# Kernel tuning notes

Measured on AMD Instinct MI355X. Metric: run time of the kernel, lower is better.

## Reference

```python
import jax, jax.numpy as jnp
import numpy as np

N = 100000      # nodes
E = 1600000     # edges
FX = 128        # raw node feature dim
MAXZ = 100      # z embedding / one-hot size
HID = 128       # hidden_channels
NL = 3          # num_layers
G = 512         # num graphs
BN_EPS = 1e-5


def _lin(key, din, dout):
    return jax.random.normal(key, (din, dout), jnp.float32) * (1.0 / np.sqrt(din))


def setup_inputs() -> dict:
    key = jax.random.key(0)
    ks = jax.random.split(key, 64)
    d = {}
    d["x"] = jax.random.normal(ks[0], (N, FX), jnp.float32)
    d["z"] = jax.random.randint(ks[1], (N,), 0, MAXZ)
    d["edge_index"] = jax.random.randint(ks[2], (2, E), 0, N)
    d["batch"] = jnp.sort(jax.random.randint(ks[3], (N,), 0, G))
    in0 = FX + 2 * MAXZ  # z_emb concatenated twice (faithful to source)
    ki = 4
    for l in range(NL):
        din = in0 if l == 0 else HID
        d[f"W1_{l}"] = _lin(ks[ki], din, HID); ki += 1
        d[f"b1_{l}"] = jnp.zeros((HID,), jnp.float32)
        d[f"W2_{l}"] = _lin(ks[ki], HID, HID); ki += 1
        d[f"b2_{l}"] = jnp.zeros((HID,), jnp.float32)
        d[f"g_{l}"] = jnp.ones((HID,), jnp.float32)
        d[f"be_{l}"] = jnp.zeros((HID,), jnp.float32)
    d["Wl1"] = _lin(ks[ki], NL * HID, HID); ki += 1
    d["bl1"] = jnp.zeros((HID,), jnp.float32)
    d["Wl2"] = _lin(ks[ki], HID, 1); ki += 1
    d["bl2"] = jnp.zeros((1,), jnp.float32)
    return d


def _gin_layer(h, src, dst, W1, b1, W2, b2, g, be):
    # GINConv with eps=0: nn(x + sum_{j->i} x_j)
    agg = jax.ops.segment_sum(h[src], dst, num_segments=N)  # [N, d]
    m = h + agg
    m = jax.nn.relu(m @ W1 + b1)
    m = jax.nn.relu(m @ W2 + b2)
    # training-mode BatchNorm1d over node axis (biased variance)
    mu = m.mean(0)
    var = jnp.mean((m - mu) ** 2, axis=0)
    return (m - mu) * jax.lax.rsqrt(var + BN_EPS) * g + be


def reference(x, z, edge_index, batch,
              W1_0, b1_0, W2_0, b2_0, g_0, be_0,
              W1_1, b1_1, W2_1, b2_1, g_1, be_1,
              W1_2, b1_2, W2_2, b2_2, g_2, be_2,
              Wl1, bl1, Wl2, bl2):
    src, dst = edge_index[0], edge_index[1]
    z_emb = jax.nn.one_hot(z, MAXZ, dtype=jnp.float32)  # [N, MAXZ]
    h = jnp.concatenate([z_emb, x], axis=1)
    h = jnp.concatenate([z_emb, h], axis=1)  # faithful double concat -> [N, FX+2*MAXZ]
    params = [(W1_0, b1_0, W2_0, b2_0, g_0, be_0),
              (W1_1, b1_1, W2_1, b2_1, g_1, be_1),
              (W1_2, b1_2, W2_2, b2_2, g_2, be_2)]
    xs = []
    for p in params:
        h = _gin_layer(h, src, dst, *p)
        xs.append(h)
    hcat = jnp.concatenate(xs, axis=1)  # jumping knowledge: [N, NL*HID]
    # global_mean_pool over graph ids
    counts = jax.ops.segment_sum(jnp.ones((N,), jnp.float32), batch, num_segments=G)
    pooled = jax.ops.segment_sum(hcat, batch, num_segments=G) / jnp.maximum(counts, 1.0)[:, None]
    out = jax.nn.relu(pooled @ Wl1 + bl1)
    # dropout is identity in eval / reference mode
    out = out @ Wl2 + bl2  # [G, 1]
    return out
```

## Files before the change

kernel.cpp:

```cpp
#include <hip/hip_runtime.h>
#include <hip/hip_bf16.h>

#define NN 100000
#define NROWS_PAD 100032
#define EE 1600000
#define GG 512
#define NPB 256
#define NB  ((NN + NPB - 1) / NPB)
#define PCHUNK 4096
#define PBLOCKS ((EE + PCHUNK - 1) / PCHUNK)
#define SBANK 8
static constexpr float BN_EPS = 1e-5f;

typedef _Float16 half8 __attribute__((ext_vector_type(8)));
typedef float floatx4 __attribute__((ext_vector_type(4)));


__global__ __launch_bounds__(256) void k_bhist(const int* __restrict__ EI,
                                               int* __restrict__ bcount)
{
    __shared__ int h[NB];
    const int t = threadIdx.x;
    for (int i = t; i < NB; i += 256) h[i] = 0;
    __syncthreads();
    const int e0 = blockIdx.x * PCHUNK;
    const int e1 = (e0 + PCHUNK < EE) ? e0 + PCHUNK : EE;
    for (int e = e0 + t; e < e1; e += 256)
        atomicAdd(&h[EI[EE + e] >> 8], 1);
    __syncthreads();
    for (int i = t; i < NB; i += 256)
        if (h[i]) atomicAdd(&bcount[i], h[i]);
}

__global__ __launch_bounds__(512) void k_bscan(const int* __restrict__ bcount,
                                               int* __restrict__ bstart,
                                               int* __restrict__ bcursor,
                                               int* __restrict__ row_start)
{
    __shared__ int s[512];
    int t = threadIdx.x;
    int v = (t < NB) ? bcount[t] : 0;
    s[t] = v;
    __syncthreads();
    for (int off = 1; off < 512; off <<= 1) {
        int u = (t >= off) ? s[t - off] : 0;
        __syncthreads();
        s[t] += u;
        __syncthreads();
    }
    if (t < NB) { int ex = s[t] - v; bstart[t] = ex; bcursor[t] = ex; }
    if (t == 0) { bstart[NB] = EE; row_start[NN] = EE; }
}

__global__ __launch_bounds__(256) void k_part(const int* __restrict__ EI,
                                              int* __restrict__ bcursor,
                                              int* __restrict__ ebuf)
{
    __shared__ int h[NB];
    __shared__ int cur[NB];
    const int t = threadIdx.x;
    for (int i = t; i < NB; i += 256) h[i] = 0;
    __syncthreads();
    const int e0 = blockIdx.x * PCHUNK;
    const int e1 = (e0 + PCHUNK < EE) ? e0 + PCHUNK : EE;
    for (int e = e0 + t; e < e1; e += 256)
        atomicAdd(&h[EI[EE + e] >> 8], 1);
    __syncthreads();
    for (int i = t; i < NB; i += 256)
        cur[i] = h[i] ? atomicAdd(&bcursor[i], h[i]) : 0;
    __syncthreads();
    for (int e = e0 + t; e < e1; e += 256) {
        int s = EI[e], d = EI[EE + e];
        int pos = atomicAdd(&cur[d >> 8], 1);
        ebuf[pos] = s | ((d & (NPB - 1)) << 17);
    }
}

__global__ __launch_bounds__(256) void k_csrbucket(const int* __restrict__ ebuf,
                                                   const int* __restrict__ bstart,
                                                   int* __restrict__ row_start,
                                                   int* __restrict__ ssrc)
{
    __shared__ int cnt[NPB];
    __shared__ int cur[NPB];
    const int b = blockIdx.x, t = threadIdx.x;
    cnt[t] = 0;
    __syncthreads();
    const int e0 = bstart[b], e1 = bstart[b + 1];
    for (int e = e0 + t; e < e1; e += 256) {
        unsigned p = (unsigned)__builtin_nontemporal_load(&ebuf[e]);
        atomicAdd(&cnt[p >> 17], 1);
    }
    __syncthreads();
    int myc = cnt[t];
    for (int off = 1; off < 256; off <<= 1) {
        int u = (t >= off) ? cnt[t - off] : 0;
        __syncthreads();
        cnt[t] += u;
        __syncthreads();
    }
    int pos0 = e0 + cnt[t] - myc;
    int idx = b * NPB + t;
    if (idx < NN) row_start[idx] = pos0;
    cur[t] = pos0;
    __syncthreads();
    for (int e = e0 + t; e < e1; e += 256) {
        unsigned p = (unsigned)__builtin_nontemporal_load(&ebuf[e]);
        int pos = atomicAdd(&cur[p >> 17], 1);
        ssrc[pos] = (int)(p & 0x1FFFFu);
    }
}


__global__ __launch_bounds__(256) void k_xcast(const float* __restrict__ X,
                                               _Float16* __restrict__ Xh)
{
    int idx = blockIdx.x * 256 + threadIdx.x;
    const float4* src = (const float4*)X;
    float4 a = src[idx * 2], b = src[idx * 2 + 1];
    half8 o = { (_Float16)a.x, (_Float16)a.y, (_Float16)a.z, (_Float16)a.w,
                (_Float16)b.x, (_Float16)b.y, (_Float16)b.z, (_Float16)b.w };
    *(half8*)&Xh[idx * 8] = o;
}

__device__ __forceinline__ void bn_sc_sh(const float* statsL,
                                         const float* g, const float* be, int k,
                                         float& sc, float& sh)
{
    float cs = 0.f, cq = 0.f;
    #pragma unroll
    for (int b = 0; b < SBANK; ++b) {
        cs += statsL[b * 256 + k];
        cq += statsL[b * 256 + 128 + k];
    }
    float inv_n = 1.0f / (float)NN;
    float mu = cs * inv_n;
    float var = cq * inv_n - mu * mu;
    sc = g[k] * rsqrtf(var + BN_EPS);
    sh = be[k] - mu * sc;
}

__global__ __launch_bounds__(256) void k_prep(
    const float* __restrict__ W1, const float* __restrict__ W2,
    const float* __restrict__ statsPrev,
    const float* __restrict__ g, const float* __restrict__ be,
    _Float16* __restrict__ Wt1, _Float16* __restrict__ Wt2,
    float* __restrict__ cvec, int l)
{
    int b = blockIdx.x, t = threadIdx.x;
    if (b < 64) {
        int idx = b * 256 + t;
        int n = idx >> 7, k = idx & 127;
        if (l == 0) {
            Wt1[idx] = (_Float16)W1[(200 + k) * 128 + n];
        } else {
            float sc, sh;
            bn_sc_sh(statsPrev, g, be, k, sc, sh);
            Wt1[idx] = (_Float16)(sc * W1[k * 128 + n]);
        }
    } else if (b < 128) {
        int idx = (b - 64) * 256 + t;
        int n = idx >> 7, k = idx & 127;
        Wt2[idx] = (_Float16)W2[k * 128 + n];
    } else if (t < 128) {
        float acc = 0.f;
        if (l != 0) {
            for (int k = 0; k < 128; ++k) {
                float sc, sh;
                bn_sc_sh(statsPrev, g, be, k, sc, sh);
                acc = fmaf(sh, W1[k * 128 + t], acc);
            }
        }
        cvec[t] = acc;
    }
}


#define MM_CORE_G(Ah, Wth)                                                   \
    const int lane = tid & 63;                                               \
    const int wv = tid >> 6;                                                 \
    const int ml = lane & 15;                                                \
    const int quad = lane >> 4;                                              \
    const int wr = wv >> 1, wc = wv & 1;                                     \
    floatx4 acc[2][4];                                                       \
    for (int r = 0; r < 2; ++r)                                              \
        for (int t = 0; t < 4; ++t)                                          \
            acc[r][t] = (floatx4){0.f, 0.f, 0.f, 0.f};                       \
    {                                                                        \
        const size_t ar0 = (size_t)(row0 + 32 * wr + ml) * 128;              \
        const size_t ar1 = ar0 + (size_t)16 * 128;                           \
        _Pragma("unroll")                                                    \
        for (int kq = 0; kq < 4; ++kq) {                                     \
            int k0 = kq * 32;                                                \
            half8 a0 = *(const half8*)&Ah[ar0 + k0 + quad * 8];              \
            half8 a1 = *(const half8*)&Ah[ar1 + k0 + quad * 8];              \
            _Pragma("unroll")                                                \
            for (int t = 0; t < 4; ++t) {                                    \
                half8 bf = *(const half8*)&Wth[(size_t)(64 * wc + 16 * t + ml) * 128 + k0 + quad * 8]; \
                acc[0][t] = __builtin_amdgcn_mfma_f32_16x16x32_f16(a0, bf, acc[0][t], 0, 0, 0); \
                acc[1][t] = __builtin_amdgcn_mfma_f32_16x16x32_f16(a1, bf, acc[1][t], 0, 0, 0); \
            }                                                                \
        }                                                                    \
    }

__global__ __launch_bounds__(256) void k_mm_embed(
    const _Float16* __restrict__ Ah, const _Float16* __restrict__ Wth,
    const int* __restrict__ Z, const float* __restrict__ W1,
    _Float16* __restrict__ Ph)
{
    const int tid = threadIdx.x;
    const int row0 = blockIdx.x * 64;
    MM_CORE_G(Ah, Wth)
    #pragma unroll
    for (int r = 0; r < 2; ++r)
        #pragma unroll
        for (int j = 0; j < 4; ++j) {
            int grow = row0 + 32 * wr + 16 * r + quad * 4 + j;
            if (grow < NN) {
                int zv = Z[grow];
                const float* w0 = &W1[zv * 128];
                const float* w1 = &W1[(100 + zv) * 128];
                #pragma unroll
                for (int t = 0; t < 4; ++t) {
                    int gcol = 64 * wc + 16 * t + ml;
                    float v = acc[r][t][j] + w0[gcol] + w1[gcol];
                    Ph[(size_t)grow * 128 + gcol] = (_Float16)v;
                }
            }
        }
}

__global__ __launch_bounds__(256) void k_mm1(
    const _Float16* __restrict__ Ah, const _Float16* __restrict__ Wth,
    _Float16* __restrict__ Ph)
{
    const int tid = threadIdx.x;
    const int row0 = blockIdx.x * 64;
    MM_CORE_G(Ah, Wth)
    #pragma unroll
    for (int r = 0; r < 2; ++r)
        #pragma unroll
        for (int j = 0; j < 4; ++j) {
            int grow = row0 + 32 * wr + 16 * r + quad * 4 + j;
            if (grow < NN) {
                #pragma unroll
                for (int t = 0; t < 4; ++t) {
                    int gcol = 64 * wc + 16 * t + ml;
                    Ph[(size_t)grow * 128 + gcol] = (_Float16)acc[r][t][j];
                }
            }
        }
}

__global__ __launch_bounds__(256) void k_mm2(
    const _Float16* __restrict__ Ah, const _Float16* __restrict__ Wth,
    const float* __restrict__ b2, _Float16* __restrict__ Oh,
    float* __restrict__ statsL)
{
    __shared__ float cs[128];
    __shared__ float cq[128];
    const int tid = threadIdx.x;
    const int row0 = blockIdx.x * 64;
    if (tid < 128) { cs[tid] = 0.f; cq[tid] = 0.f; }
    __syncthreads();

    MM_CORE_G(Ah, Wth)

    float b2v[4];
    #pragma unroll
    for (int t = 0; t < 4; ++t) b2v[t] = b2[64 * wc + 16 * t + ml];
    float st[4] = {0.f, 0.f, 0.f, 0.f};
    float qt[4] = {0.f, 0.f, 0.f, 0.f};
    #pragma unroll
    for (int r = 0; r < 2; ++r)
        #pragma unroll
        for (int j = 0; j < 4; ++j) {
            int grow = row0 + 32 * wr + 16 * r + quad * 4 + j;
            if (grow < NN) {
                #pragma unroll
                for (int t = 0; t < 4; ++t) {
                    int gcol = 64 * wc + 16 * t + ml;
                    float v = fmaxf(acc[r][t][j] + b2v[t], 0.f);
                    Oh[(size_t)grow * 128 + gcol] = (_Float16)v;
                    st[t] += v;
                    qt[t] += v * v;
                }
            }
        }
    #pragma unroll
    for (int t = 0; t < 4; ++t) {
        int gcol = 64 * wc + 16 * t + ml;
        atomicAdd(&cs[gcol], st[t]);
        atomicAdd(&cq[gcol], qt[t]);
    }
    __syncthreads();
    if (tid < 128) {
        float* bank = statsL + (blockIdx.x & (SBANK - 1)) * 256;
        atomicAdd(&bank[tid], cs[tid]);
        atomicAdd(&bank[128 + tid], cq[tid]);
    }
}


__global__ __launch_bounds__(256) void k_aggregate(
    const _Float16* __restrict__ Ph, const int* __restrict__ row_start,
    const int* __restrict__ ssrc, const float* __restrict__ b1,
    const float* __restrict__ cvec, _Float16* __restrict__ Mh)
{
    int idx = blockIdx.x * 256 + threadIdx.x;
    int node = idx >> 4, q = idx & 15;
    if (node >= NN) return;
    int s0 = row_start[node], s1 = row_start[node + 1];
    float degp1 = (float)(s1 - s0 + 1);
    float acc[8];
    half8 pv = *(const half8*)&Ph[(size_t)node * 128 + q * 8];
    #pragma unroll
    for (int j = 0; j < 8; ++j)
        acc[j] = (float)pv[j] + fmaf(degp1, cvec[q * 8 + j], b1[q * 8 + j]);
    int e = s0;
    for (; e + 7 < s1; e += 8) {
        int sidx[8];
        #pragma unroll
        for (int u = 0; u < 8; ++u)
            sidx[u] = __builtin_nontemporal_load(&ssrc[e + u]);
        half8 v[8];
        #pragma unroll
        for (int u = 0; u < 8; ++u)
            v[u] = *(const half8*)&Ph[(size_t)sidx[u] * 128 + q * 8];
        #pragma unroll
        for (int j = 0; j < 8; ++j)
            acc[j] += (((float)v[0][j] + (float)v[1][j]) + ((float)v[2][j] + (float)v[3][j]))
                    + (((float)v[4][j] + (float)v[5][j]) + ((float)v[6][j] + (float)v[7][j]));
    }
    for (; e + 1 < s1; e += 2) {
        int sa = __builtin_nontemporal_load(&ssrc[e]);
        int sb = __builtin_nontemporal_load(&ssrc[e + 1]);
        half8 va = *(const half8*)&Ph[(size_t)sa * 128 + q * 8];
        half8 vb = *(const half8*)&Ph[(size_t)sb * 128 + q * 8];
        #pragma unroll
        for (int j = 0; j < 8; ++j) acc[j] += (float)va[j] + (float)vb[j];
    }
    if (e < s1) {
        int sa = __builtin_nontemporal_load(&ssrc[e]);
        half8 va = *(const half8*)&Ph[(size_t)sa * 128 + q * 8];
        #pragma unroll
        for (int j = 0; j < 8; ++j) acc[j] += (float)va[j];
    }
    half8 o;
    #pragma unroll
    for (int j = 0; j < 8; ++j) o[j] = (_Float16)fmaxf(acc[j], 0.f);
    __builtin_nontemporal_store(o, (half8*)&Mh[(size_t)node * 128 + q * 8]);
}


__global__ __launch_bounds__(128) void k_pool(
    const _Float16* __restrict__ Ah, const int* __restrict__ batch,
    const float* __restrict__ statsL,
    const float* __restrict__ g_, const float* __restrict__ be,
    float* __restrict__ pooled, int loff)
{
    __shared__ float red[8][128];
    int g = blockIdx.x;
    int t = threadIdx.x;
    int rg = t >> 4, seg = t & 15;
    int lo = 0, hi = NN;
    while (lo < hi) { int mid = (lo + hi) >> 1; if (batch[mid] < g) lo = mid + 1; else hi = mid; }
    int s = lo;
    lo = s; hi = NN;
    while (lo < hi) { int mid = (lo + hi) >> 1; if (batch[mid] < g + 1) lo = mid + 1; else hi = mid; }
    int e = lo;
    float acc[8] = {};
    for (int i = s + rg; i < e; i += 8) {
        half8 v = *(const half8*)&Ah[(size_t)i * 128 + seg * 8];
        #pragma unroll
        for (int j = 0; j < 8; ++j) acc[j] += (float)v[j];
    }
    #pragma unroll
    for (int j = 0; j < 8; ++j) red[rg][seg * 8 + j] = acc[j];
    __syncthreads();
    int cnt = e - s;
    float inv = 1.0f / (float)(cnt > 0 ? cnt : 1);
    if (t < 128) {
        float s_ = 0.f;
        #pragma unroll
        for (int r = 0; r < 8; ++r) s_ += red[r][t];
        float sc, sh;
        bn_sc_sh(statsL, g_, be, t, sc, sh);
        pooled[g * 384 + loff + t] = fmaf(sc, s_ * inv, sh);
    }
}

__global__ __launch_bounds__(128) void k_final(
    const float* __restrict__ pooled,
    const float* __restrict__ Wl1, const float* __restrict__ bl1,
    const float* __restrict__ Wl2, const float* __restrict__ bl2,
    float* __restrict__ out)
{
    __shared__ float pr[384];
    __shared__ float red[128];
    int g = blockIdx.x, j = threadIdx.x;
    for (int i = j; i < 384; i += 128) pr[i] = pooled[g * 384 + i];
    __syncthreads();
    float acc = bl1[j];
    for (int k = 0; k < 384; ++k) acc = fmaf(pr[k], Wl1[k * 128 + j], acc);
    float r = fmaxf(acc, 0.f) * Wl2[j];
    red[j] = r;
    __syncthreads();
    for (int off = 64; off > 0; off >>= 1) {
        if (j < off) red[j] += red[j + off];
        __syncthreads();
    }
    if (j == 0) out[g] = red[0] + bl2[0];
}

extern "C" void kernel_launch(void* const* d_in, const int* in_sizes, int n_in,
                              void* d_out, int out_size, void* d_ws, size_t ws_size,
                              hipStream_t stream)
{
    const float* x     = (const float*)d_in[0];
    const int*   z     = (const int*)d_in[1];
    const int*   ei    = (const int*)d_in[2];
    const int*   batch = (const int*)d_in[3];
    const float* W1a[3] = {(const float*)d_in[4],  (const float*)d_in[10], (const float*)d_in[16]};
    const float* b1a[3] = {(const float*)d_in[5],  (const float*)d_in[11], (const float*)d_in[17]};
    const float* W2a[3] = {(const float*)d_in[6],  (const float*)d_in[12], (const float*)d_in[18]};
    const float* b2a[3] = {(const float*)d_in[7],  (const float*)d_in[13], (const float*)d_in[19]};
    const float* ga[3]  = {(const float*)d_in[8],  (const float*)d_in[14], (const float*)d_in[20]};
    const float* bea[3] = {(const float*)d_in[9],  (const float*)d_in[15], (const float*)d_in[21]};
    const float* Wl1 = (const float*)d_in[22];
    const float* bl1 = (const float*)d_in[23];
    const float* Wl2 = (const float*)d_in[24];
    const float* bl2 = (const float*)d_in[25];
    float* out = (float*)d_out;

    char* ws = (char*)d_ws;
    size_t off = 0;
    auto alloc = [&](size_t bytes) {
        void* p = ws + off;
        off += (bytes + 255) & ~(size_t)255;
        return p;
    };
    _Float16* Xh  = (_Float16*)alloc((size_t)NROWS_PAD * 128 * 2);
    _Float16* Ph  = (_Float16*)alloc((size_t)NROWS_PAD * 128 * 2);
    _Float16* Mh  = (_Float16*)alloc((size_t)NROWS_PAD * 128 * 2);
    _Float16* Ahb = (_Float16*)alloc((size_t)NROWS_PAD * 128 * 2);
    _Float16* Wt1 = (_Float16*)alloc((size_t)128 * 128 * 2);
    _Float16* Wt2 = (_Float16*)alloc((size_t)128 * 128 * 2);
    int*   ebuf     = (int*)alloc((size_t)EE * 4);
    int*   ssrc     = (int*)alloc((size_t)EE * 4);
    int*   row_st   = (int*)alloc((size_t)(NN + 1) * 4);
    int*   bcount   = (int*)alloc((size_t)NB * 4);
    int*   bstart   = (int*)alloc((size_t)(NB + 1) * 4);
    int*   bcursor  = (int*)alloc((size_t)NB * 4);
    float* cvec     = (float*)alloc(128 * 4);
    float* stats    = (float*)alloc((size_t)3 * SBANK * 256 * 4);
    float* pooled   = (float*)alloc((size_t)GG * 384 * 4);

    const int gemmBlocks = (NN + 63) / 64;
    const int aggBlocks  = (NN * 16 + 255) / 256;

    hipMemsetAsync(stats, 0, (size_t)3 * SBANK * 256 * 4, stream);
    hipMemsetAsync(bcount, 0, (size_t)NB * 4, stream);
    k_xcast<<<(NN * 128 / 8 + 255) / 256, 256, 0, stream>>>(x, Xh);
    k_bhist<<<PBLOCKS, 256, 0, stream>>>(ei, bcount);
    k_bscan<<<1, 512, 0, stream>>>(bcount, bstart, bcursor, row_st);
    k_part<<<PBLOCKS, 256, 0, stream>>>(ei, bcursor, ebuf);
    k_csrbucket<<<NB, 256, 0, stream>>>(ebuf, bstart, row_st, ssrc);

    for (int l = 0; l < 3; ++l) {
        float* statsL   = stats + (size_t)l * SBANK * 256;
        const float* statsPrev = (l > 0) ? stats + (size_t)(l - 1) * SBANK * 256 : stats;
        const float* pg   = (l > 0) ? ga[l - 1] : ga[0];
        const float* pbe  = (l > 0) ? bea[l - 1] : bea[0];
        k_prep<<<129, 256, 0, stream>>>(W1a[l], W2a[l], statsPrev, pg, pbe,
                                        Wt1, Wt2, cvec, l);
        if (l == 0)
            k_mm_embed<<<gemmBlocks, 256, 0, stream>>>(Xh, Wt1, z, W1a[0], Ph);
        else
            k_mm1<<<gemmBlocks, 256, 0, stream>>>(Ahb, Wt1, Ph);
        k_aggregate<<<aggBlocks, 256, 0, stream>>>(Ph, row_st, ssrc, b1a[l], cvec, Mh);
        k_mm2<<<gemmBlocks, 256, 0, stream>>>(Mh, Wt2, b2a[l], Ahb, statsL);
        k_pool<<<GG, 128, 0, stream>>>(Ahb, batch, statsL, ga[l], bea[l],
                                       pooled, l * 128);
    }
    k_final<<<GG, 128, 0, stream>>>(pooled, Wl1, bl1, Wl2, bl2, out);
}
```

Before: 706.5 us.

## Sort nodes by degree for aggregation and unroll gathers by sixteen with prefetch

Adds a counting sort of nodes by in-degree (histogram, scan, scatter) once per call and makes the aggregate kernel process nodes in that permuted order, so wavefronts hold nodes of similar degree and suffer less divergence. The gather loop also gains a 16-wide main loop that prefetches the next batch of source indices while the current feature rows load, raising memory-level parallelism. The cost is three extra small kernels, an indirection through perm, scattered rather than sequential node order for row reads and Mh writes, and higher register pressure under launch_bounds(256,4).

```diff
diff --git a/kernel.cpp b/kernel.cpp
--- a/kernel.cpp
+++ b/kernel.cpp
@@ -10,6 +10,7 @@
 #define PCHUNK 4096
 #define PBLOCKS ((EE + PCHUNK - 1) / PCHUNK)
 #define SBANK 8
+#define DBINS 64
 static constexpr float BN_EPS = 1e-5f;
 
 typedef _Float16 half8 __attribute__((ext_vector_type(8)));
@@ -109,6 +110,63 @@
         int pos = atomicAdd(&cur[p >> 17], 1);
         ssrc[pos] = (int)(p & 0x1FFFFu);
     }
+}
+
+
+__global__ __launch_bounds__(256) void k_deghist(const int* __restrict__ row_start,
+                                                 int* __restrict__ dhist)
+{
+    __shared__ int h[DBINS];
+    int t = threadIdx.x;
+    if (t < DBINS) h[t] = 0;
+    __syncthreads();
+    int i = blockIdx.x * 256 + t;
+    if (i < NN) {
+        int d = row_start[i + 1] - row_start[i];
+        if (d >= DBINS) d = DBINS - 1;
+        atomicAdd(&h[d], 1);
+    }
+    __syncthreads();
+    if (t < DBINS && h[t]) atomicAdd(&dhist[t], h[t]);
+}
+
+__global__ __launch_bounds__(64) void k_degscan(const int* __restrict__ dhist,
+                                                int* __restrict__ dcur)
+{
+    __shared__ int s[DBINS];
+    int t = threadIdx.x;
+    int v = dhist[t];
+    s[t] = v;
+    __syncthreads();
+    for (int off = 1; off < DBINS; off <<= 1) {
+        int u = (t >= off) ? s[t - off] : 0;
+        __syncthreads();
+        s[t] += u;
+        __syncthreads();
+    }
+    dcur[t] = s[t] - v;
+}
+
+__global__ __launch_bounds__(256) void k_degscatter(const int* __restrict__ row_start,
+                                                    int* __restrict__ dcur,
+                                                    int* __restrict__ perm)
+{
+    __shared__ int h[DBINS];
+    __shared__ int base[DBINS];
+    int t = threadIdx.x;
+    if (t < DBINS) h[t] = 0;
+    __syncthreads();
+    int i = blockIdx.x * 256 + t;
+    int d = 0, lpos = 0;
+    if (i < NN) {
+        d = row_start[i + 1] - row_start[i];
+        if (d >= DBINS) d = DBINS - 1;
+        lpos = atomicAdd(&h[d], 1);
+    }
+    __syncthreads();
+    if (t < DBINS && h[t]) base[t] = atomicAdd(&dcur[t], h[t]);
+    __syncthreads();
+    if (i < NN) perm[base[d] + lpos] = i;
 }
 
 
@@ -302,14 +360,26 @@
 }
 
 
-__global__ __launch_bounds__(256) void k_aggregate(
+#define ACCUM16(v)                                                            \
+    _Pragma("unroll")                                                         \
+    for (int j = 0; j < 8; ++j) {                                             \
+        float t0 = (((float)v[0][j] + (float)v[1][j]) + ((float)v[2][j] + (float)v[3][j]));   \
+        float t1 = (((float)v[4][j] + (float)v[5][j]) + ((float)v[6][j] + (float)v[7][j]));   \
+        float t2 = (((float)v[8][j] + (float)v[9][j]) + ((float)v[10][j] + (float)v[11][j])); \
+        float t3 = (((float)v[12][j] + (float)v[13][j]) + ((float)v[14][j] + (float)v[15][j]));\
+        acc[j] += (t0 + t1) + (t2 + t3);                                      \
+    }
+
+__global__ __launch_bounds__(256, 4) void k_aggregate(
     const _Float16* __restrict__ Ph, const int* __restrict__ row_start,
     const int* __restrict__ ssrc, const float* __restrict__ b1,
-    const float* __restrict__ cvec, _Float16* __restrict__ Mh)
+    const float* __restrict__ cvec, const int* __restrict__ perm,
+    _Float16* __restrict__ Mh)
 {
     int idx = blockIdx.x * 256 + threadIdx.x;
-    int node = idx >> 4, q = idx & 15;
-    if (node >= NN) return;
+    int slot = idx >> 4, q = idx & 15;
+    if (slot >= NN) return;
+    int node = perm[slot];
     int s0 = row_start[node], s1 = row_start[node + 1];
     float degp1 = (float)(s1 - s0 + 1);
     float acc[8];
@@ -317,7 +387,34 @@
     #pragma unroll
     for (int j = 0; j < 8; ++j)
         acc[j] = (float)pv[j] + fmaf(degp1, cvec[q * 8 + j], b1[q * 8 + j]);
+
     int e = s0;
+    int nfull = (s1 - s0) >> 4;
+    if (nfull > 0) {
+        int sidx[16];
+        #pragma unroll
+        for (int u = 0; u < 16; ++u)
+            sidx[u] = __builtin_nontemporal_load(&ssrc[e + u]);
+        for (int b = 0; b < nfull - 1; ++b) {
+            half8 v[16];
+            #pragma unroll
+            for (int u = 0; u < 16; ++u)
+                v[u] = *(const half8*)&Ph[(size_t)sidx[u] * 128 + q * 8];
+            #pragma unroll
+            for (int u = 0; u < 16; ++u)
+                sidx[u] = __builtin_nontemporal_load(&ssrc[e + 16 + u]);
+            ACCUM16(v)
+            e += 16;
+        }
+        {
+            half8 v[16];
+            #pragma unroll
+            for (int u = 0; u < 16; ++u)
+                v[u] = *(const half8*)&Ph[(size_t)sidx[u] * 128 + q * 8];
+            ACCUM16(v)
+            e += 16;
+        }
+    }
     for (; e + 7 < s1; e += 8) {
         int sidx[8];
         #pragma unroll
@@ -452,6 +549,9 @@
     int*   bcount   = (int*)alloc((size_t)NB * 4);
     int*   bstart   = (int*)alloc((size_t)(NB + 1) * 4);
     int*   bcursor  = (int*)alloc((size_t)NB * 4);
+    int*   dhist    = (int*)alloc((size_t)DBINS * 4);
+    int*   dcur     = (int*)alloc((size_t)DBINS * 4);
+    int*   perm     = (int*)alloc((size_t)NN * 4);
     float* cvec     = (float*)alloc(128 * 4);
     float* stats    = (float*)alloc((size_t)3 * SBANK * 256 * 4);
     float* pooled   = (float*)alloc((size_t)GG * 384 * 4);
@@ -461,11 +561,15 @@
 
     hipMemsetAsync(stats, 0, (size_t)3 * SBANK * 256 * 4, stream);
     hipMemsetAsync(bcount, 0, (size_t)NB * 4, stream);
+    hipMemsetAsync(dhist, 0, (size_t)DBINS * 4, stream);
     k_xcast<<<(NN * 128 / 8 + 255) / 256, 256, 0, stream>>>(x, Xh);
     k_bhist<<<PBLOCKS, 256, 0, stream>>>(ei, bcount);
     k_bscan<<<1, 512, 0, stream>>>(bcount, bstart, bcursor, row_st);
     k_part<<<PBLOCKS, 256, 0, stream>>>(ei, bcursor, ebuf);
     k_csrbucket<<<NB, 256, 0, stream>>>(ebuf, bstart, row_st, ssrc);
+    k_deghist<<<(NN + 255) / 256, 256, 0, stream>>>(row_st, dhist);
+    k_degscan<<<1, DBINS, 0, stream>>>(dhist, dcur);
+    k_degscatter<<<(NN + 255) / 256, 256, 0, stream>>>(row_st, dcur, perm);
 
     for (int l = 0; l < 3; ++l) {
         float* statsL   = stats + (size_t)l * SBANK * 256;
@@ -478,7 +582,7 @@
             k_mm_embed<<<gemmBlocks, 256, 0, stream>>>(Xh, Wt1, z, W1a[0], Ph);
         else
             k_mm1<<<gemmBlocks, 256, 0, stream>>>(Ahb, Wt1, Ph);
-        k_aggregate<<<aggBlocks, 256, 0, stream>>>(Ph, row_st, ssrc, b1a[l], cvec, Mh);
+        k_aggregate<<<aggBlocks, 256, 0, stream>>>(Ph, row_st, ssrc, b1a[l], cvec, perm, Mh);
         k_mm2<<<gemmBlocks, 256, 0, stream>>>(Mh, Wt2, b2a[l], Ahb, statsL);
         k_pool<<<GG, 128, 0, stream>>>(Ahb, batch, statsL, ga[l], bea[l],
                                        pooled, l * 128);
```

New measurement: 720.3 us. About the same (+2.0%).

## Fuse neighbor aggregation into second GEMM and fold fp32-to-fp16 cast into embed GEMM

Applied to the files above, without the earlier changes.

Merges the edge-gather aggregation kernel with the second MLP GEMM. Each block aggregates 64 nodes into an XOR-swizzled shared-memory tile and then runs MFMA on that tile, so the intermediate M buffer no longer goes through global memory. It also drops the separate x cast kernel by converting fp32 x to fp16 inside the layer-0 GEMM's operand loads. The risks are lower parallelism in the gather phase, since 256 threads loop over 4 node groups serially, and the extra shared memory limiting occupancy.

```diff
diff --git a/kernel.cpp b/kernel.cpp
--- a/kernel.cpp
+++ b/kernel.cpp
@@ -111,17 +111,6 @@
     }
 }
 
-
-__global__ __launch_bounds__(256) void k_xcast(const float* __restrict__ X,
-                                               _Float16* __restrict__ Xh)
-{
-    int idx = blockIdx.x * 256 + threadIdx.x;
-    const float4* src = (const float4*)X;
-    float4 a = src[idx * 2], b = src[idx * 2 + 1];
-    half8 o = { (_Float16)a.x, (_Float16)a.y, (_Float16)a.z, (_Float16)a.w,
-                (_Float16)b.x, (_Float16)b.y, (_Float16)b.z, (_Float16)b.w };
-    *(half8*)&Xh[idx * 8] = o;
-}
 
 __device__ __forceinline__ void bn_sc_sh(const float* statsL,
                                          const float* g, const float* be, int k,
@@ -204,13 +193,47 @@
     }
 
 __global__ __launch_bounds__(256) void k_mm_embed(
-    const _Float16* __restrict__ Ah, const _Float16* __restrict__ Wth,
+    const float* __restrict__ X, const _Float16* __restrict__ Wth,
     const int* __restrict__ Z, const float* __restrict__ W1,
     _Float16* __restrict__ Ph)
 {
     const int tid = threadIdx.x;
     const int row0 = blockIdx.x * 64;
-    MM_CORE_G(Ah, Wth)
+    const int lane = tid & 63;
+    const int wv = tid >> 6;
+    const int ml = lane & 15;
+    const int quad = lane >> 4;
+    const int wr = wv >> 1, wc = wv & 1;
+    floatx4 acc[2][4];
+    #pragma unroll
+    for (int r = 0; r < 2; ++r)
+        #pragma unroll
+        for (int t = 0; t < 4; ++t)
+            acc[r][t] = (floatx4){0.f, 0.f, 0.f, 0.f};
+    int r0g = row0 + 32 * wr + ml;
+    int r1g = r0g + 16;
+    if (r0g > NN - 1) r0g = NN - 1;
+    if (r1g > NN - 1) r1g = NN - 1;
+    const float* x0 = &X[(size_t)r0g * 128];
+    const float* x1 = &X[(size_t)r1g * 128];
+    #pragma unroll
+    for (int kq = 0; kq < 4; ++kq) {
+        int k0 = kq * 32 + quad * 8;
+        float4 f0a = *(const float4*)&x0[k0];
+        float4 f0b = *(const float4*)&x0[k0 + 4];
+        float4 f1a = *(const float4*)&x1[k0];
+        float4 f1b = *(const float4*)&x1[k0 + 4];
+        half8 a0 = { (_Float16)f0a.x, (_Float16)f0a.y, (_Float16)f0a.z, (_Float16)f0a.w,
+                     (_Float16)f0b.x, (_Float16)f0b.y, (_Float16)f0b.z, (_Float16)f0b.w };
+        half8 a1 = { (_Float16)f1a.x, (_Float16)f1a.y, (_Float16)f1a.z, (_Float16)f1a.w,
+                     (_Float16)f1b.x, (_Float16)f1b.y, (_Float16)f1b.z, (_Float16)f1b.w };
+        #pragma unroll
+        for (int t = 0; t < 4; ++t) {
+            half8 bf = *(const half8*)&Wth[(size_t)(64 * wc + 16 * t + ml) * 128 + kq * 32 + quad * 8];
+            acc[0][t] = __builtin_amdgcn_mfma_f32_16x16x32_f16(a0, bf, acc[0][t], 0, 0, 0);
+            acc[1][t] = __builtin_amdgcn_mfma_f32_16x16x32_f16(a1, bf, acc[1][t], 0, 0, 0);
+        }
+    }
     #pragma unroll
     for (int r = 0; r < 2; ++r)
         #pragma unroll
@@ -252,19 +275,98 @@
         }
 }
 
-__global__ __launch_bounds__(256) void k_mm2(
-    const _Float16* __restrict__ Ah, const _Float16* __restrict__ Wth,
+
+__global__ __launch_bounds__(256) void k_aggmm2(
+    const _Float16* __restrict__ Ph, const int* __restrict__ row_start,
+    const int* __restrict__ ssrc, const float* __restrict__ b1,
+    const float* __restrict__ cvec, const _Float16* __restrict__ Wth,
     const float* __restrict__ b2, _Float16* __restrict__ Oh,
     float* __restrict__ statsL)
 {
+    __shared__ _Float16 Msh[64 * 128];
     __shared__ float cs[128];
     __shared__ float cq[128];
     const int tid = threadIdx.x;
     const int row0 = blockIdx.x * 64;
     if (tid < 128) { cs[tid] = 0.f; cq[tid] = 0.f; }
-    __syncthreads();
-
-    MM_CORE_G(Ah, Wth)
+
+    const int grp = tid >> 4, q = tid & 15;
+    #pragma unroll 1
+    for (int n = 0; n < 4; ++n) {
+        const int r = (n << 4) + grp;
+        const int node = row0 + r;
+        float acc[8] = {0.f, 0.f, 0.f, 0.f, 0.f, 0.f, 0.f, 0.f};
+        if (node < NN) {
+            int s0 = row_start[node], s1 = row_start[node + 1];
+            float degp1 = (float)(s1 - s0 + 1);
+            half8 pv = *(const half8*)&Ph[(size_t)node * 128 + q * 8];
+            #pragma unroll
+            for (int j = 0; j < 8; ++j)
+                acc[j] = (float)pv[j] + fmaf(degp1, cvec[q * 8 + j], b1[q * 8 + j]);
+            int e = s0;
+            for (; e + 7 < s1; e += 8) {
+                int sidx[8];
+                #pragma unroll
+                for (int u = 0; u < 8; ++u)
+                    sidx[u] = __builtin_nontemporal_load(&ssrc[e + u]);
+                half8 v[8];
+                #pragma unroll
+                for (int u = 0; u < 8; ++u)
+                    v[u] = *(const half8*)&Ph[(size_t)sidx[u] * 128 + q * 8];
+                #pragma unroll
+                for (int j = 0; j < 8; ++j)
+                    acc[j] += (((float)v[0][j] + (float)v[1][j]) + ((float)v[2][j] + (float)v[3][j]))
+                            + (((float)v[4][j] + (float)v[5][j]) + ((float)v[6][j] + (float)v[7][j]));
+            }
+            for (; e + 1 < s1; e += 2) {
+                int sa = __builtin_nontemporal_load(&ssrc[e]);
+                int sb = __builtin_nontemporal_load(&ssrc[e + 1]);
+                half8 va = *(const half8*)&Ph[(size_t)sa * 128 + q * 8];
+                half8 vb = *(const half8*)&Ph[(size_t)sb * 128 + q * 8];
+                #pragma unroll
+                for (int j = 0; j < 8; ++j) acc[j] += (float)va[j] + (float)vb[j];
+            }
+            if (e < s1) {
+                int sa = __builtin_nontemporal_load(&ssrc[e]);
+                half8 va = *(const half8*)&Ph[(size_t)sa * 128 + q * 8];
+                #pragma unroll
+                for (int j = 0; j < 8; ++j) acc[j] += (float)va[j];
+            }
+        }
+        half8 o;
+        #pragma unroll
+        for (int j = 0; j < 8; ++j) o[j] = (_Float16)fmaxf(acc[j], 0.f);
+        const int colsw = (q * 8) ^ ((r & 15) * 8);
+        *(half8*)&Msh[r * 128 + colsw] = o;
+    }
+    __syncthreads();
+
+    const int lane = tid & 63;
+    const int wv = tid >> 6;
+    const int ml = lane & 15;
+    const int quad = lane >> 4;
+    const int wr = wv >> 1, wc = wv & 1;
+    floatx4 acc2[2][4];
+    #pragma unroll
+    for (int r = 0; r < 2; ++r)
+        #pragma unroll
+        for (int t = 0; t < 4; ++t)
+            acc2[r][t] = (floatx4){0.f, 0.f, 0.f, 0.f};
+    const int r0 = 32 * wr + ml;
+    const int xorm = ml * 8;
+    #pragma unroll
+    for (int kq = 0; kq < 4; ++kq) {
+        int k0 = kq * 32;
+        int c0 = k0 + quad * 8;
+        half8 a0 = *(const half8*)&Msh[r0 * 128 + (c0 ^ xorm)];
+        half8 a1 = *(const half8*)&Msh[(r0 + 16) * 128 + (c0 ^ xorm)];
+        #pragma unroll
+        for (int t = 0; t < 4; ++t) {
+            half8 bf = *(const half8*)&Wth[(size_t)(64 * wc + 16 * t + ml) * 128 + k0 + quad * 8];
+            acc2[0][t] = __builtin_amdgcn_mfma_f32_16x16x32_f16(a0, bf, acc2[0][t], 0, 0, 0);
+            acc2[1][t] = __builtin_amdgcn_mfma_f32_16x16x32_f16(a1, bf, acc2[1][t], 0, 0, 0);
+        }
+    }
 
     float b2v[4];
     #pragma unroll
@@ -280,7 +382,7 @@
                 #pragma unroll
                 for (int t = 0; t < 4; ++t) {
                     int gcol = 64 * wc + 16 * t + ml;
-                    float v = fmaxf(acc[r][t][j] + b2v[t], 0.f);
+                    float v = fmaxf(acc2[r][t][j] + b2v[t], 0.f);
                     Oh[(size_t)grow * 128 + gcol] = (_Float16)v;
                     st[t] += v;
                     qt[t] += v * v;
@@ -299,57 +401,6 @@
         atomicAdd(&bank[tid], cs[tid]);
         atomicAdd(&bank[128 + tid], cq[tid]);
     }
-}
-
-
-__global__ __launch_bounds__(256) void k_aggregate(
-    const _Float16* __restrict__ Ph, const int* __restrict__ row_start,
-    const int* __restrict__ ssrc, const float* __restrict__ b1,
-    const float* __restrict__ cvec, _Float16* __restrict__ Mh)
-{
-    int idx = blockIdx.x * 256 + threadIdx.x;
-    int node = idx >> 4, q = idx & 15;
-    if (node >= NN) return;
-    int s0 = row_start[node], s1 = row_start[node + 1];
-    float degp1 = (float)(s1 - s0 + 1);
-    float acc[8];
-    half8 pv = *(const half8*)&Ph[(size_t)node * 128 + q * 8];
-    #pragma unroll
-    for (int j = 0; j < 8; ++j)
-        acc[j] = (float)pv[j] + fmaf(degp1, cvec[q * 8 + j], b1[q * 8 + j]);
-    int e = s0;
-    for (; e + 7 < s1; e += 8) {
-        int sidx[8];
-        #pragma unroll
-        for (int u = 0; u < 8; ++u)
-            sidx[u] = __builtin_nontemporal_load(&ssrc[e + u]);
-        half8 v[8];
-        #pragma unroll
-        for (int u = 0; u < 8; ++u)
-            v[u] = *(const half8*)&Ph[(size_t)sidx[u] * 128 + q * 8];
-        #pragma unroll
-        for (int j = 0; j < 8; ++j)
-            acc[j] += (((float)v[0][j] + (float)v[1][j]) + ((float)v[2][j] + (float)v[3][j]))
-                    + (((float)v[4][j] + (float)v[5][j]) + ((float)v[6][j] + (float)v[7][j]));
-    }
-    for (; e + 1 < s1; e += 2) {
-        int sa = __builtin_nontemporal_load(&ssrc[e]);
-        int sb = __builtin_nontemporal_load(&ssrc[e + 1]);
-        half8 va = *(const half8*)&Ph[(size_t)sa * 128 + q * 8];
-        half8 vb = *(const half8*)&Ph[(size_t)sb * 128 + q * 8];
-        #pragma unroll
-        for (int j = 0; j < 8; ++j) acc[j] += (float)va[j] + (float)vb[j];
-    }
-    if (e < s1) {
-        int sa = __builtin_nontemporal_load(&ssrc[e]);
-        half8 va = *(const half8*)&Ph[(size_t)sa * 128 + q * 8];
-        #pragma unroll
-        for (int j = 0; j < 8; ++j) acc[j] += (float)va[j];
-    }
-    half8 o;
-    #pragma unroll
-    for (int j = 0; j < 8; ++j) o[j] = (_Float16)fmaxf(acc[j], 0.f);
-    __builtin_nontemporal_store(o, (half8*)&Mh[(size_t)node * 128 + q * 8]);
 }
 
 
@@ -440,9 +491,7 @@
         off += (bytes + 255) & ~(size_t)255;
         return p;
     };
-    _Float16* Xh  = (_Float16*)alloc((size_t)NROWS_PAD * 128 * 2);
     _Float16* Ph  = (_Float16*)alloc((size_t)NROWS_PAD * 128 * 2);
-    _Float16* Mh  = (_Float16*)alloc((size_t)NROWS_PAD * 128 * 2);
     _Float16* Ahb = (_Float16*)alloc((size_t)NROWS_PAD * 128 * 2);
     _Float16* Wt1 = (_Float16*)alloc((size_t)128 * 128 * 2);
     _Float16* Wt2 = (_Float16*)alloc((size_t)128 * 128 * 2);
@@ -457,11 +506,9 @@
     float* pooled   = (float*)alloc((size_t)GG * 384 * 4);
 
     const int gemmBlocks = (NN + 63) / 64;
-    const int aggBlocks  = (NN * 16 + 255) / 256;
 
     hipMemsetAsync(stats, 0, (size_t)3 * SBANK * 256 * 4, stream);
     hipMemsetAsync(bcount, 0, (size_t)NB * 4, stream);
-    k_xcast<<<(NN * 128 / 8 + 255) / 256, 256, 0, stream>>>(x, Xh);
     k_bhist<<<PBLOCKS, 256, 0, stream>>>(ei, bcount);
     k_bscan<<<1, 512, 0, stream>>>(bcount, bstart, bcursor, row_st);
     k_part<<<PBLOCKS, 256, 0, stream>>>(ei, bcursor, ebuf);
@@ -475,11 +522,11 @@
         k_prep<<<129, 256, 0, stream>>>(W1a[l], W2a[l], statsPrev, pg, pbe,
                                         Wt1, Wt2, cvec, l);
         if (l == 0)
-            k_mm_embed<<<gemmBlocks, 256, 0, stream>>>(Xh, Wt1, z, W1a[0], Ph);
+            k_mm_embed<<<gemmBlocks, 256, 0, stream>>>(x, Wt1, z, W1a[0], Ph);
         else
             k_mm1<<<gemmBlocks, 256, 0, stream>>>(Ahb, Wt1, Ph);
-        k_aggregate<<<aggBlocks, 256, 0, stream>>>(Ph, row_st, ssrc, b1a[l], cvec, Mh);
-        k_mm2<<<gemmBlocks, 256, 0, stream>>>(Mh, Wt2, b2a[l], Ahb, statsL);
+        k_aggmm2<<<gemmBlocks, 256, 0, stream>>>(Ph, row_st, ssrc, b1a[l], cvec,
+                                                 Wt2, b2a[l], Ahb, statsL);
         k_pool<<<GG, 128, 0, stream>>>(Ahb, batch, statsL, ga[l], bea[l],
                                        pooled, l * 128);
     }
```

Result: no change. 712.8 us (+0.9%).
